# Optimization experiments

Hardware: AMD Instinct MI355X
Metric: run time of the kernel (lower is better)

Reference implementation:

```python
import jax, jax.numpy as jnp
import numpy as np

B, T, D = 2, 4096, 1024      # batch, seq, hidden_dim
E, I = 16, 512               # n_routed_experts, expert_intermediate
K = 2                        # n_activated_experts
IS = 2048                    # shared_expert_intermediate
ALPHA = 1e-4                 # balance_loss_alpha
EPS = 1e-9


def setup_inputs() -> dict:
    key = jax.random.key(0)
    ks = jax.random.split(key, 8)
    s = lambda k, shape, fan: jax.random.normal(k, shape, jnp.float32) * (fan ** -0.5)
    return {
        "x": jax.random.normal(ks[0], (B, T, D), jnp.float32),
        "gate_w": s(ks[1], (D, E), D),            # router gate (no bias)
        "expert_bias": jnp.zeros((E,), jnp.float32),
        "sh_gate": s(ks[2], (D, IS), D),          # shared expert SwiGLU
        "sh_up": s(ks[3], (D, IS), D),
        "sh_down": s(ks[4], (IS, D), IS),
        "ex_gate": s(ks[5], (E, D, I), D),        # routed experts (stacked)
        "ex_up": s(ks[6], (E, D, I), D),
        "ex_down": s(ks[7], (E, I, D), I),
    }


def _swiglu(x, wg, wu, wd):
    return (jax.nn.silu(x @ wg) * (x @ wu)) @ wd


def reference(x, gate_w, expert_bias, sh_gate, sh_up, sh_down, ex_gate, ex_up, ex_down):
    Bq, Tq, Dq = x.shape
    # shared expert path (n_shared_experts = 1)
    shared = _swiglu(x, sh_gate, sh_up, sh_down)

    xf = x.reshape(Bq * Tq, Dq)                       # (N, D)
    N = xf.shape[0]

    # --- router: sigmoid gating, bias-adjusted top-k, normalized gates ---
    affinity = jax.nn.sigmoid(xf @ gate_w)            # (N, E)
    scores = affinity + expert_bias[None, :]
    _, idx = jax.lax.top_k(scores, K)                 # (N, K) int
    gv = jnp.take_along_axis(affinity, idx, axis=1)   # (N, K) gathered from affinity
    gv = gv / (gv.sum(-1, keepdims=True) + EPS)

    # --- balance loss (sequence-wise, Eq. 17-20) ---
    expert_mask = jax.nn.one_hot(idx, E, dtype=jnp.float32).sum(1)  # (N, E)
    f = expert_mask.sum(0) * E / (K * N)
    P = (affinity / (affinity.sum(-1, keepdims=True) + EPS)).mean(0)
    balance_loss = ALPHA * (f * P).sum()
    expert_counts = expert_mask.sum(0).astype(jnp.int32)            # (E,)

    # --- dispatch/compute/combine, expressed as dense combine-weight matrix ---
    # w[n, e] = sum of gate values for token n routed to expert e (same math
    # as the masked gather/scatter loop in the original)
    w = jnp.zeros((N, E), jnp.float32).at[jnp.arange(N)[:, None], idx].add(gv)
    h = jax.nn.silu(jnp.einsum('nd,edi->eni', xf, ex_gate)) \
        * jnp.einsum('nd,edi->eni', xf, ex_up)        # (E, N, I)
    routed = jnp.einsum('ne,eni,eid->nd', w, h, ex_down)  # (N, D)
    routed = routed.reshape(Bq, Tq, Dq)

    output = shared + routed  # note: original does NOT add residual despite docstring
    return output, balance_loss, expert_counts
```

## Files before the change

kernel.cpp:

```cpp
#include <hip/hip_runtime.h>
#include <stdint.h>

#define NTOK 8192
#define DDIM 1024
#define NEXP 16
#define KSEL 2
#define ISH 2048
#define IEX 512
#define ALPHAC 1e-4f
#define REPS 1e-9f

typedef __attribute__((ext_vector_type(8))) short short8;
typedef __attribute__((ext_vector_type(4))) float f32x4;

__device__ __forceinline__ unsigned short f2bf(float f){
  union { float f; uint32_t u; } v; v.f = f;
  uint32_t u = v.u;
  uint32_t r = (u + 0x7fffu + ((u >> 16) & 1u)) >> 16;
  return (unsigned short)r;
}
__device__ __forceinline__ float bf2f(unsigned short h){
  union { uint32_t u; float f; } v; v.u = ((uint32_t)h) << 16; return v.f;
}

__device__ __forceinline__ void gload16(const void* g, void* l){
  __builtin_amdgcn_global_load_lds(
      (const __attribute__((address_space(1))) void*)g,
      (__attribute__((address_space(3))) void*)l, 16, 0, 0);
}

__global__ __launch_bounds__(256) void convert_f32_bf16(const float* __restrict__ in,
                                                        unsigned short* __restrict__ out){
  int id = blockIdx.x * 256 + threadIdx.x;
  float4 v = ((const float4*)in)[id];
  ushort4 o;
  o.x = f2bf(v.x); o.y = f2bf(v.y); o.z = f2bf(v.z); o.w = f2bf(v.w);
  ((ushort4*)out)[id] = o;
}

__global__ __launch_bounds__(256) void transpose_bf16(const float* __restrict__ in,
                                                      unsigned short* __restrict__ outp,
                                                      int R, int C){
  __shared__ float tile[64][65];
  const size_t bofs = (size_t)blockIdx.z * R * C;
  const float* ip = in + bofs;
  unsigned short* op = outp + bofs;
  int c0 = blockIdx.x * 64, r0 = blockIdx.y * 64;
  int t = threadIdx.x;
  int tr = t >> 4, tc = (t & 15) * 4;
  #pragma unroll
  for (int i = 0; i < 4; ++i){
    float4 v = *(const float4*)&ip[(size_t)(r0 + tr + i*16) * C + c0 + tc];
    tile[tr + i*16][tc+0] = v.x;
    tile[tr + i*16][tc+1] = v.y;
    tile[tr + i*16][tc+2] = v.z;
    tile[tr + i*16][tc+3] = v.w;
  }
  __syncthreads();
  #pragma unroll
  for (int i = 0; i < 4; ++i){
    int oc = tr + i*16;
    ushort4 w;
    w.x = f2bf(tile[tc+0][oc]);
    w.y = f2bf(tile[tc+1][oc]);
    w.z = f2bf(tile[tc+2][oc]);
    w.w = f2bf(tile[tc+3][oc]);
    *(ushort4*)&op[(size_t)(c0 + oc) * R + r0 + tc] = w;
  }
}

__global__ __launch_bounds__(256) void logits_kernel(
    const float* __restrict__ x, const float* __restrict__ gw,
    float* __restrict__ logits)
{
  __shared__ float gws[16][1024];
  const int t = threadIdx.x;
  #pragma unroll
  for (int k = 0; k < 16; ++k){
    int idx = t + k * 256;
    float4 v = ((const float4*)gw)[idx];
    int d = idx >> 2, e0 = (idx & 3) * 4;
    gws[e0+0][d] = v.x;
    gws[e0+1][d] = v.y;
    gws[e0+2][d] = v.z;
    gws[e0+3][d] = v.w;
  }
  __syncthreads();
  const int lane = t & 63, w = t >> 6;
  const int nb = blockIdx.x * 16 + w * 4;
  for (int i = 0; i < 4; ++i){
    const int n = nb + i;
    const float4* xr = (const float4*)(x + (size_t)n * DDIM);
    float4 xv[4];
    #pragma unroll
    for (int k = 0; k < 4; ++k) xv[k] = xr[lane + k*64];
    float acc[16];
    #pragma unroll
    for (int e = 0; e < 16; ++e){
      float s = 0.f;
      #pragma unroll
      for (int k = 0; k < 4; ++k){
        float4 g = *(const float4*)&gws[e][(lane + k*64)*4];
        s = fmaf(xv[k].x, g.x, fmaf(xv[k].y, g.y, fmaf(xv[k].z, g.z, fmaf(xv[k].w, g.w, s))));
      }
      acc[e] = s;
    }
    #pragma unroll
    for (int m = 1; m < 64; m <<= 1)
      #pragma unroll
      for (int e = 0; e < 16; ++e)
        acc[e] += __shfl_xor(acc[e], m);
    if (lane == 0){
      float4* op = (float4*)(logits + (size_t)n * 16);
      op[0] = make_float4(acc[0],  acc[1],  acc[2],  acc[3]);
      op[1] = make_float4(acc[4],  acc[5],  acc[6],  acc[7]);
      op[2] = make_float4(acc[8],  acc[9],  acc[10], acc[11]);
      op[3] = make_float4(acc[12], acc[13], acc[14], acc[15]);
    }
  }
}

__global__ __launch_bounds__(256) void router_finish(
    const float* __restrict__ logits, const float* __restrict__ ebias,
    int* __restrict__ idxb, float* __restrict__ gvb,
    float* __restrict__ Ppart, int* __restrict__ Cpart)
{
  __shared__ float Ps[16];
  __shared__ int Cs[16];
  const int t = threadIdx.x;
  if (t < 16){ Ps[t] = 0.f; Cs[t] = 0; }
  __syncthreads();
  const int lane = t & 63;
  const int n = blockIdx.x * 256 + t;
  const float4* lp = (const float4*)(logits + (size_t)n * 16);
  float4 a0 = lp[0], a1 = lp[1], a2 = lp[2], a3 = lp[3];
  float aff[16];
  aff[0]=a0.x; aff[1]=a0.y; aff[2]=a0.z; aff[3]=a0.w;
  aff[4]=a1.x; aff[5]=a1.y; aff[6]=a1.z; aff[7]=a1.w;
  aff[8]=a2.x; aff[9]=a2.y; aff[10]=a2.z; aff[11]=a2.w;
  aff[12]=a3.x; aff[13]=a3.y; aff[14]=a3.z; aff[15]=a3.w;
  float rowsum = REPS;
  #pragma unroll
  for (int e = 0; e < 16; ++e){
    aff[e] = 1.f / (1.f + __expf(-aff[e]));
    rowsum += aff[e];
  }
  float bj[16];
  #pragma unroll
  for (int e = 0; e < 16; ++e) bj[e] = ebias[e];
  float bestS = aff[0] + bj[0], bestA = aff[0]; int i1 = 0;
  #pragma unroll
  for (int j = 1; j < 16; ++j){
    float sc = aff[j] + bj[j];
    bool gt2 = sc > bestS;
    bestS = gt2 ? sc : bestS; bestA = gt2 ? aff[j] : bestA; i1 = gt2 ? j : i1;
  }
  float secS = -1e30f, secA = 0.f; int i2 = 0;
  #pragma unroll
  for (int j = 0; j < 16; ++j){
    float sc = aff[j] + bj[j];
    bool ok = (j != i1) && (sc > secS);
    secS = ok ? sc : secS; secA = ok ? aff[j] : secA; i2 = ok ? j : i2;
  }
  float den = bestA + secA + REPS;
  idxb[n*2]   = i1; idxb[n*2+1] = i2;
  gvb[n*2]    = bestA / den; gvb[n*2+1] = secA / den;

  float inv = 1.f / rowsum;
  float pv[16]; int cv[16];
  #pragma unroll
  for (int e = 0; e < 16; ++e){
    pv[e] = aff[e] * inv;
    cv[e] = (e == i1) + (e == i2);
  }
  #pragma unroll
  for (int m = 1; m < 64; m <<= 1)
    #pragma unroll
    for (int e = 0; e < 16; ++e){
      pv[e] += __shfl_xor(pv[e], m);
      cv[e] += __shfl_xor(cv[e], m);
    }
  if (lane == 0){
    #pragma unroll
    for (int e = 0; e < 16; ++e){
      atomicAdd(&Ps[e], pv[e]);
      atomicAdd(&Cs[e], cv[e]);
    }
  }
  __syncthreads();
  if (t < 16){ Ppart[blockIdx.x*16 + t] = Ps[t]; Cpart[blockIdx.x*16 + t] = Cs[t]; }
}

__global__ __launch_bounds__(256) void finalize2(
    const float* __restrict__ Ppart, const int* __restrict__ Cpart,
    int* __restrict__ counts, int* __restrict__ offs, int* __restrict__ cursor,
    float* __restrict__ out_tail)
{
  __shared__ float P[16];
  __shared__ int C[16];
  int t = threadIdx.x;
  if (t < 16){ P[t] = 0.f; C[t] = 0; }
  __syncthreads();
  if (t < 32){
    int e = t & 15, c = t >> 4;
    float p = 0.f; int cc = 0;
    for (int b = c * 16; b < c * 16 + 16; ++b){ p += Ppart[b*16 + e]; cc += Cpart[b*16 + e]; }
    atomicAdd(&P[e], p); atomicAdd(&C[e], cc);
  }
  __syncthreads();
  if (t == 0){
    int a = 0; float loss = 0.f;
    for (int i = 0; i < 16; ++i){
      offs[i] = a; cursor[i] = a; counts[i] = C[i]; a += C[i];
      loss += ((float)C[i] * (float)NEXP / (float)(KSEL * NTOK)) * (P[i] / (float)NTOK);
      out_tail[1+i] = (float)C[i];
    }
    out_tail[0] = ALPHAC * loss;
  }
}

__global__ __launch_bounds__(256) void slot_assign(
    const int* __restrict__ idxb, const float* __restrict__ gvb,
    int* __restrict__ cursor, int* __restrict__ tokp, float* __restrict__ gatep,
    int* __restrict__ rslot)
{
  int i = blockIdx.x * 256 + threadIdx.x;
  int e = idxb[i];
  int s = atomicAdd(&cursor[e], 1);
  tokp[s] = i >> 1;
  gatep[s] = gvb[i];
  rslot[i] = s;
}

template<bool GROUPED, bool GATHER, int MODE>
__global__ __launch_bounds__(256, 2) void gemm128(
    const unsigned short* __restrict__ A,
    const unsigned short* __restrict__ B,
    const unsigned short* __restrict__ comp,
    void* __restrict__ Cout,
    int M, int N, int K,
    const int* __restrict__ counts,
    const int* __restrict__ offsets,
    const int* __restrict__ perm,
    const float* __restrict__ rowscale)
{
  __shared__ __align__(16) unsigned short As[2][128*64];
  __shared__ __align__(16) unsigned short Bs[2][128*64];

  const int bx = blockIdx.x, by = blockIdx.y;
  int mt = bx, off = 0, cnt = M;
  const unsigned short* bp = B;
  if (GROUPED){
    int acc = 0, e = -1;
    #pragma unroll
    for (int i = 0; i < NEXP; ++i){
      int c = counts[i]; int tt = (c + 127) >> 7;
      if (e < 0 && bx < acc + tt){ e = i; mt = bx - acc; off = offsets[i]; cnt = c; }
      acc += tt;
    }
    if (e < 0) return;
    bp += (size_t)e * N * K;
  }
  const int m0 = mt * 128, n0 = by * 128;
  const int t = threadIdx.x;
  const int lane = t & 63;
  const int wid = t >> 6;
  const int wm = (wid >> 1) * 64;
  const int wn = (wid & 1) * 64;
  const int l15 = lane & 15, g = lane >> 4;

  const unsigned short* asrc[4];
  const unsigned short* bsrc[4];
  int ldso[4];
  #pragma unroll
  for (int c = 0; c < 4; ++c){
    int s = (wid*4 + c)*64 + lane;
    int row = s >> 3, c16 = s & 7;
    int scol = (c16 ^ (row & 7)) * 8;
    ldso[c] = (wid*4 + c) * 512;
    int r = m0 + row;
    int rc = GROUPED ? (r < cnt ? r : (cnt > 0 ? cnt - 1 : 0)) : r;
    int ar;
    if (GATHER) ar = perm[off + rc];
    else        ar = GROUPED ? off + rc : rc;
    asrc[c] = A + (size_t)ar * K + scol;
    bsrc[c] = bp + (size_t)(n0 + row) * K + scol;
  }

  f32x4 acc[4][4];
  #pragma unroll
  for (int i = 0; i < 4; ++i)
    #pragma unroll
    for (int j = 0; j < 4; ++j)
      #pragma unroll
      for (int r = 0; r < 4; ++r) acc[i][j][r] = 0.f;

  auto STAGE = [&](int buf, int k0){
    #pragma unroll
    for (int c = 0; c < 4; ++c) gload16(asrc[c] + k0, (void*)&As[buf][ldso[c]]);
    #pragma unroll
    for (int c = 0; c < 4; ++c) gload16(bsrc[c] + k0, (void*)&Bs[buf][ldso[c]]);
  };

  const int nt = K >> 6;
  STAGE(0, 0);
  __syncthreads();
  int cur = 0;
  for (int tk = 0; tk < nt; ++tk){
    if (tk + 1 < nt) STAGE(cur ^ 1, (tk + 1) << 6);
    #pragma unroll
    for (int ks = 0; ks < 2; ++ks){
      short8 af[4], bf[4];
      #pragma unroll
      for (int i = 0; i < 4; ++i){
        int row = wm + i * 16 + l15;
        af[i] = *(const short8*)&As[cur][row * 64 + (((ks*4 + g) ^ (row & 7)) * 8)];
      }
      #pragma unroll
      for (int j = 0; j < 4; ++j){
        int row = wn + j * 16 + l15;
        bf[j] = *(const short8*)&Bs[cur][row * 64 + (((ks*4 + g) ^ (row & 7)) * 8)];
      }
      #pragma unroll
      for (int i = 0; i < 4; ++i)
        #pragma unroll
        for (int j = 0; j < 4; ++j)
          acc[i][j] = __builtin_amdgcn_mfma_f32_16x16x32_bf16(af[i], bf[j], acc[i][j], 0, 0, 0);
    }
    __syncthreads();
    cur ^= 1;
  }

  #pragma unroll
  for (int i = 0; i < 4; ++i)
    #pragma unroll
    for (int j = 0; j < 4; ++j)
      #pragma unroll
      for (int r = 0; r < 4; ++r){
        int lr = wm + i * 16 + g * 4 + r;
        int grow = m0 + lr;
        if (GROUPED && grow >= cnt) continue;
        int gcol = n0 + wn + j * 16 + l15;
        size_t orow = GROUPED ? (size_t)(off + grow) : (size_t)grow;
        float val = acc[i][j][r];
        if (MODE == 1){
          ((float*)Cout)[orow * N + gcol] = val;
        } else {
          if (MODE == 2) val *= rowscale[off + grow];
          if (MODE == 4) val = val / (1.f + __expf(-val));
          if (MODE == 5) val *= bf2f(comp[orow * N + gcol]);
          ((unsigned short*)Cout)[orow * N + gcol] = f2bf(val);
        }
      }
}

__global__ __launch_bounds__(256) void combine_kernel(float* __restrict__ out,
                                                      const unsigned short* __restrict__ ybuf,
                                                      const int* __restrict__ rs){
  int id = blockIdx.x * 256 + threadIdx.x;
  int n = id >> 8;
  int q = id & 255;
  int s0 = rs[n*2], s1 = rs[n*2+1];
  float4 o = ((float4*)out)[id];
  ushort4 a = ((const ushort4*)(ybuf + (size_t)s0 * DDIM))[q];
  ushort4 b = ((const ushort4*)(ybuf + (size_t)s1 * DDIM))[q];
  o.x += bf2f(a.x) + bf2f(b.x);
  o.y += bf2f(a.y) + bf2f(b.y);
  o.z += bf2f(a.z) + bf2f(b.z);
  o.w += bf2f(a.w) + bf2f(b.w);
  ((float4*)out)[id] = o;
}

extern "C" void kernel_launch(void* const* d_in, const int* in_sizes, int n_in,
                              void* d_out, int out_size, void* d_ws, size_t ws_size,
                              hipStream_t stream)
{
  const float* x       = (const float*)d_in[0];
  const float* gate_w  = (const float*)d_in[1];
  const float* ebias   = (const float*)d_in[2];
  const float* sh_gate = (const float*)d_in[3];
  const float* sh_up   = (const float*)d_in[4];
  const float* sh_down = (const float*)d_in[5];
  const float* ex_gate = (const float*)d_in[6];
  const float* ex_up   = (const float*)d_in[7];
  const float* ex_down = (const float*)d_in[8];
  float* out = (float*)d_out;
  (void)in_sizes; (void)n_in; (void)out_size; (void)ws_size;

  size_t o = 0;
  auto alloc = [&](size_t bytes) -> void* {
    o = (o + 255) & ~(size_t)255;
    void* p = (char*)d_ws + o;
    o += bytes;
    return p;
  };
  unsigned short* xb   = (unsigned short*)alloc((size_t)NTOK*DDIM*2);
  unsigned short* shgT = (unsigned short*)alloc((size_t)ISH*DDIM*2);
  unsigned short* shuT = (unsigned short*)alloc((size_t)ISH*DDIM*2);
  unsigned short* shdT = (unsigned short*)alloc((size_t)DDIM*ISH*2);
  unsigned short* exgT = (unsigned short*)alloc((size_t)NEXP*IEX*DDIM*2);
  unsigned short* exuT = (unsigned short*)alloc((size_t)NEXP*IEX*DDIM*2);
  unsigned short* exdT = (unsigned short*)alloc((size_t)NEXP*DDIM*IEX*2);
  unsigned short* hbuf = (unsigned short*)alloc((size_t)NTOK*KSEL*IEX*2);
  unsigned short* big  = (unsigned short*)alloc((size_t)NTOK*ISH*2);
  float* logits = (float*)alloc((size_t)NTOK*NEXP*4);
  int*   idxb  = (int*)alloc(NTOK*KSEL*4);
  float* gvb   = (float*)alloc(NTOK*KSEL*4);
  float* Ppart = (float*)alloc(32*16*4);
  int*   Cpart = (int*)alloc(32*16*4);
  int*   counts= (int*)alloc(64);
  int*   offs  = (int*)alloc(64);
  int*   cursor= (int*)alloc(64);
  int*   tokp  = (int*)alloc(NTOK*KSEL*4);
  float* gatep = (float*)alloc(NTOK*KSEL*4);
  int*   rslot = (int*)alloc(NTOK*KSEL*4);

  convert_f32_bf16<<<NTOK*DDIM/1024, 256, 0, stream>>>(x, xb);
  transpose_bf16<<<dim3(ISH/64,  DDIM/64, 1),    256, 0, stream>>>(sh_gate, shgT, DDIM, ISH);
  transpose_bf16<<<dim3(ISH/64,  DDIM/64, 1),    256, 0, stream>>>(sh_up,   shuT, DDIM, ISH);
  transpose_bf16<<<dim3(DDIM/64, ISH/64,  1),    256, 0, stream>>>(sh_down, shdT, ISH, DDIM);
  transpose_bf16<<<dim3(IEX/64,  DDIM/64, NEXP), 256, 0, stream>>>(ex_gate, exgT, DDIM, IEX);
  transpose_bf16<<<dim3(IEX/64,  DDIM/64, NEXP), 256, 0, stream>>>(ex_up,   exuT, DDIM, IEX);
  transpose_bf16<<<dim3(DDIM/64, IEX/64,  NEXP), 256, 0, stream>>>(ex_down, exdT, IEX, DDIM);

  logits_kernel<<<512, 256, 0, stream>>>(x, gate_w, logits);
  router_finish<<<32, 256, 0, stream>>>(logits, ebias, idxb, gvb, Ppart, Cpart);
  finalize2<<<1, 256, 0, stream>>>(Ppart, Cpart, counts, offs, cursor,
                                   out + (size_t)NTOK*DDIM);
  slot_assign<<<NTOK*KSEL/256, 256, 0, stream>>>(idxb, gvb, cursor, tokp, gatep, rslot);

  gemm128<false,false,4><<<dim3(NTOK/128, ISH/128), 256, 0, stream>>>(
      xb, shgT, nullptr, big, NTOK, ISH, DDIM, nullptr, nullptr, nullptr, nullptr);
  gemm128<false,false,5><<<dim3(NTOK/128, ISH/128), 256, 0, stream>>>(
      xb, shuT, big, big, NTOK, ISH, DDIM, nullptr, nullptr, nullptr, nullptr);
  gemm128<false,false,1><<<dim3(NTOK/128, DDIM/128), 256, 0, stream>>>(
      big, shdT, nullptr, out, NTOK, DDIM, ISH, nullptr, nullptr, nullptr, nullptr);

  gemm128<true,true,4><<<dim3(144, IEX/128), 256, 0, stream>>>(
      xb, exgT, nullptr, hbuf, 0, IEX, DDIM, counts, offs, tokp, nullptr);
  gemm128<true,true,5><<<dim3(144, IEX/128), 256, 0, stream>>>(
      xb, exuT, hbuf, hbuf, 0, IEX, DDIM, counts, offs, tokp, nullptr);
  gemm128<true,false,2><<<dim3(144, DDIM/128), 256, 0, stream>>>(
      hbuf, exdT, nullptr, big, 0, DDIM, IEX, counts, offs, nullptr, gatep);

  combine_kernel<<<NTOK*DDIM/1024, 256, 0, stream>>>(out, big, rslot);
}
```

Measured before the change: 458.2 us.

## Fuse routed gate/up GEMMs via interleaved weights and remap workgroups across XCDs

Routed expert gate and up weights are transposed into one interleaved buffer (gate and up rows alternate), so a single grouped GEMM computes both. Its epilogue pairs adjacent columns with a lane shuffle and writes silu(gate)*up directly. This removes one GEMM launch, one re-read of the gathered activations, and the hbuf round-trip. All GEMMs also switch to a 1D grid with an XCD-aware block remap (bid&7 striding) to improve L2 locality. The cost is that half the lanes sit idle in the fused epilogue's stores.

```diff
diff --git a/kernel.cpp b/kernel.cpp
--- a/kernel.cpp
+++ b/kernel.cpp
@@ -38,13 +38,13 @@
   ((ushort4*)out)[id] = o;
 }
 
+template<int RM, int RO>
 __global__ __launch_bounds__(256) void transpose_bf16(const float* __restrict__ in,
                                                       unsigned short* __restrict__ outp,
                                                       int R, int C){
   __shared__ float tile[64][65];
-  const size_t bofs = (size_t)blockIdx.z * R * C;
-  const float* ip = in + bofs;
-  unsigned short* op = outp + bofs;
+  const float* ip = in + (size_t)blockIdx.z * R * C;
+  unsigned short* op = outp + (size_t)blockIdx.z * R * C * RM;
   int c0 = blockIdx.x * 64, r0 = blockIdx.y * 64;
   int t = threadIdx.x;
   int tr = t >> 4, tc = (t & 15) * 4;
@@ -65,7 +65,7 @@
     w.y = f2bf(tile[tc+1][oc]);
     w.z = f2bf(tile[tc+2][oc]);
     w.w = f2bf(tile[tc+3][oc]);
-    *(ushort4*)&op[(size_t)(c0 + oc) * R + r0 + tc] = w;
+    *(ushort4*)&op[(size_t)((c0 + oc) * RM + RO) * R + r0 + tc] = w;
   }
 }
 
@@ -232,7 +232,7 @@
   rslot[i] = s;
 }
 
-template<bool GROUPED, bool GATHER, int MODE>
+template<bool GROUPED, bool GATHER, int MODE, int NYT>
 __global__ __launch_bounds__(256, 2) void gemm128(
     const unsigned short* __restrict__ A,
     const unsigned short* __restrict__ B,
@@ -247,21 +247,26 @@
   __shared__ __align__(16) unsigned short As[2][128*64];
   __shared__ __align__(16) unsigned short Bs[2][128*64];
 
-  const int bx = blockIdx.x, by = blockIdx.y;
-  int mt = bx, off = 0, cnt = M;
+  const int nwg = gridDim.x;
+  const int bid = blockIdx.x;
+  const int wg = (bid & 7) * (nwg >> 3) + (bid >> 3);
+  const int mtl = wg / NYT;
+  const int nt  = wg % NYT;
+
+  int mt = mtl, off = 0, cnt = M;
   const unsigned short* bp = B;
   if (GROUPED){
     int acc = 0, e = -1;
     #pragma unroll
     for (int i = 0; i < NEXP; ++i){
       int c = counts[i]; int tt = (c + 127) >> 7;
-      if (e < 0 && bx < acc + tt){ e = i; mt = bx - acc; off = offsets[i]; cnt = c; }
+      if (e < 0 && mtl < acc + tt){ e = i; mt = mtl - acc; off = offsets[i]; cnt = c; }
       acc += tt;
     }
     if (e < 0) return;
     bp += (size_t)e * N * K;
   }
-  const int m0 = mt * 128, n0 = by * 128;
+  const int m0 = mt * 128, n0 = nt * 128;
   const int t = threadIdx.x;
   const int lane = t & 63;
   const int wid = t >> 6;
@@ -302,12 +307,12 @@
     for (int c = 0; c < 4; ++c) gload16(bsrc[c] + k0, (void*)&Bs[buf][ldso[c]]);
   };
 
-  const int nt = K >> 6;
+  const int ntk = K >> 6;
   STAGE(0, 0);
   __syncthreads();
   int cur = 0;
-  for (int tk = 0; tk < nt; ++tk){
-    if (tk + 1 < nt) STAGE(cur ^ 1, (tk + 1) << 6);
+  for (int tk = 0; tk < ntk; ++tk){
+    if (tk + 1 < ntk) STAGE(cur ^ 1, (tk + 1) << 6);
     #pragma unroll
     for (int ks = 0; ks < 2; ++ks){
       short8 af[4], bf[4];
@@ -345,6 +350,12 @@
         float val = acc[i][j][r];
         if (MODE == 1){
           ((float*)Cout)[orow * N + gcol] = val;
+        } else if (MODE == 6){
+          float uo = __shfl_xor(val, 1);
+          if (!(l15 & 1)){
+            float rv = val / (1.f + __expf(-val)) * uo;
+            ((unsigned short*)Cout)[orow * (N >> 1) + (gcol >> 1)] = f2bf(rv);
+          }
         } else {
           if (MODE == 2) val *= rowscale[off + grow];
           if (MODE == 4) val = val / (1.f + __expf(-val));
@@ -394,15 +405,14 @@
     o += bytes;
     return p;
   };
-  unsigned short* xb   = (unsigned short*)alloc((size_t)NTOK*DDIM*2);
-  unsigned short* shgT = (unsigned short*)alloc((size_t)ISH*DDIM*2);
-  unsigned short* shuT = (unsigned short*)alloc((size_t)ISH*DDIM*2);
-  unsigned short* shdT = (unsigned short*)alloc((size_t)DDIM*ISH*2);
-  unsigned short* exgT = (unsigned short*)alloc((size_t)NEXP*IEX*DDIM*2);
-  unsigned short* exuT = (unsigned short*)alloc((size_t)NEXP*IEX*DDIM*2);
-  unsigned short* exdT = (unsigned short*)alloc((size_t)NEXP*DDIM*IEX*2);
-  unsigned short* hbuf = (unsigned short*)alloc((size_t)NTOK*KSEL*IEX*2);
-  unsigned short* big  = (unsigned short*)alloc((size_t)NTOK*ISH*2);
+  unsigned short* xb    = (unsigned short*)alloc((size_t)NTOK*DDIM*2);
+  unsigned short* shgT  = (unsigned short*)alloc((size_t)ISH*DDIM*2);
+  unsigned short* shuT  = (unsigned short*)alloc((size_t)ISH*DDIM*2);
+  unsigned short* shdT  = (unsigned short*)alloc((size_t)DDIM*ISH*2);
+  unsigned short* exguT = (unsigned short*)alloc((size_t)NEXP*2*IEX*DDIM*2);
+  unsigned short* exdT  = (unsigned short*)alloc((size_t)NEXP*DDIM*IEX*2);
+  unsigned short* hbuf  = (unsigned short*)alloc((size_t)NTOK*KSEL*IEX*2);
+  unsigned short* big   = (unsigned short*)alloc((size_t)NTOK*ISH*2);
   float* logits = (float*)alloc((size_t)NTOK*NEXP*4);
   int*   idxb  = (int*)alloc(NTOK*KSEL*4);
   float* gvb   = (float*)alloc(NTOK*KSEL*4);
@@ -416,12 +426,12 @@
   int*   rslot = (int*)alloc(NTOK*KSEL*4);
 
   convert_f32_bf16<<<NTOK*DDIM/1024, 256, 0, stream>>>(x, xb);
-  transpose_bf16<<<dim3(ISH/64,  DDIM/64, 1),    256, 0, stream>>>(sh_gate, shgT, DDIM, ISH);
-  transpose_bf16<<<dim3(ISH/64,  DDIM/64, 1),    256, 0, stream>>>(sh_up,   shuT, DDIM, ISH);
-  transpose_bf16<<<dim3(DDIM/64, ISH/64,  1),    256, 0, stream>>>(sh_down, shdT, ISH, DDIM);
-  transpose_bf16<<<dim3(IEX/64,  DDIM/64, NEXP), 256, 0, stream>>>(ex_gate, exgT, DDIM, IEX);
-  transpose_bf16<<<dim3(IEX/64,  DDIM/64, NEXP), 256, 0, stream>>>(ex_up,   exuT, DDIM, IEX);
-  transpose_bf16<<<dim3(DDIM/64, IEX/64,  NEXP), 256, 0, stream>>>(ex_down, exdT, IEX, DDIM);
+  transpose_bf16<1,0><<<dim3(ISH/64,  DDIM/64, 1),    256, 0, stream>>>(sh_gate, shgT, DDIM, ISH);
+  transpose_bf16<1,0><<<dim3(ISH/64,  DDIM/64, 1),    256, 0, stream>>>(sh_up,   shuT, DDIM, ISH);
+  transpose_bf16<1,0><<<dim3(DDIM/64, ISH/64,  1),    256, 0, stream>>>(sh_down, shdT, ISH, DDIM);
+  transpose_bf16<2,0><<<dim3(IEX/64,  DDIM/64, NEXP), 256, 0, stream>>>(ex_gate, exguT, DDIM, IEX);
+  transpose_bf16<2,1><<<dim3(IEX/64,  DDIM/64, NEXP), 256, 0, stream>>>(ex_up,   exguT, DDIM, IEX);
+  transpose_bf16<1,0><<<dim3(DDIM/64, IEX/64,  NEXP), 256, 0, stream>>>(ex_down, exdT, IEX, DDIM);
 
   logits_kernel<<<512, 256, 0, stream>>>(x, gate_w, logits);
   router_finish<<<32, 256, 0, stream>>>(logits, ebias, idxb, gvb, Ppart, Cpart);
@@ -429,18 +439,16 @@
                                    out + (size_t)NTOK*DDIM);
   slot_assign<<<NTOK*KSEL/256, 256, 0, stream>>>(idxb, gvb, cursor, tokp, gatep, rslot);
 
-  gemm128<false,false,4><<<dim3(NTOK/128, ISH/128), 256, 0, stream>>>(
+  gemm128<false,false,4,16><<<64*16, 256, 0, stream>>>(
       xb, shgT, nullptr, big, NTOK, ISH, DDIM, nullptr, nullptr, nullptr, nullptr);
-  gemm128<false,false,5><<<dim3(NTOK/128, ISH/128), 256, 0, stream>>>(
+  gemm128<false,false,5,16><<<64*16, 256, 0, stream>>>(
       xb, shuT, big, big, NTOK, ISH, DDIM, nullptr, nullptr, nullptr, nullptr);
-  gemm128<false,false,1><<<dim3(NTOK/128, DDIM/128), 256, 0, stream>>>(
+  gemm128<false,false,1,8><<<64*8, 256, 0, stream>>>(
       big, shdT, nullptr, out, NTOK, DDIM, ISH, nullptr, nullptr, nullptr, nullptr);
 
-  gemm128<true,true,4><<<dim3(144, IEX/128), 256, 0, stream>>>(
-      xb, exgT, nullptr, hbuf, 0, IEX, DDIM, counts, offs, tokp, nullptr);
-  gemm128<true,true,5><<<dim3(144, IEX/128), 256, 0, stream>>>(
-      xb, exuT, hbuf, hbuf, 0, IEX, DDIM, counts, offs, tokp, nullptr);
-  gemm128<true,false,2><<<dim3(144, DDIM/128), 256, 0, stream>>>(
+  gemm128<true,true,6,8><<<144*8, 256, 0, stream>>>(
+      xb, exguT, nullptr, hbuf, 0, 2*IEX, DDIM, counts, offs, tokp, nullptr);
+  gemm128<true,false,2,8><<<144*8, 256, 0, stream>>>(
       hbuf, exdT, nullptr, big, 0, DDIM, IEX, counts, offs, nullptr, gatep);
 
   combine_kernel<<<NTOK*DDIM/1024, 256, 0, stream>>>(out, big, rslot);
```

Result: faster. 413.0 us (-9.9%).
